# Optimization experiments

Hardware: AMD Instinct MI355X
Metric: run time of the kernel (lower is better)

Reference implementation:

```python
import jax, jax.numpy as jnp
import numpy as np
from jax import lax

PATCH = 4
EMBED = 96


def setup_inputs() -> dict:
    key = jax.random.key(0)
    k1, k2, k3, k4, k5 = jax.random.split(key, 5)
    rgb = jax.random.normal(k1, (8, 3, 512, 512), dtype=jnp.float32)
    hs = jax.random.normal(k2, (8, 4, 512, 512), dtype=jnp.float32)
    dem = jax.random.normal(k3, (8, 1, 512, 512), dtype=jnp.float32)
    W = jax.random.normal(k4, (EMBED, 1, PATCH, PATCH), dtype=jnp.float32) * 0.05
    b = jax.random.normal(k5, (EMBED,), dtype=jnp.float32) * 0.05
    return {"rgb": rgb, "hs": hs, "dem": dem, "W": W, "b": b}


def reference(rgb, hs, dem, W, b):
    # Concatenate modalities along channel dim: [B, C=8, H, Wd]
    x = jnp.concatenate([rgb, hs, dem], axis=1)
    B, C, H, Wd = x.shape
    # Pad H, W up to a multiple of patch size (right/bottom), as in _padding
    pad_h = (-H) % PATCH
    pad_w = (-Wd) % PATCH
    if pad_h or pad_w:
        x = jnp.pad(x, ((0, 0), (0, 0), (0, pad_h), (0, pad_w)))
    H2, W2 = x.shape[2], x.shape[3]
    # Each channel goes through the SAME 1->embed_dim conv; fold channels into batch
    xc = x.reshape(B * C, 1, H2, W2)
    y = lax.conv_general_dilated(
        xc, W,
        window_strides=(PATCH, PATCH),
        padding='VALID',
        dimension_numbers=('NCHW', 'OIHW', 'NCHW'),
    ) + b[None, :, None, None]
    Hp, Wp = y.shape[2], y.shape[3]
    # Unfold back and concat per-channel embeddings along channel dim: [B, C*embed, Hp, Wp]
    y = y.reshape(B, C * EMBED, Hp, Wp)
    return y
```

## Files before the change

### kernel.cpp

```cpp
#include <hip/hip_runtime.h>
#include <hip/hip_bf16.h>

#define PATCH 4
#define EMBED 96
#define HIN 512
#define WIN 512
#define HP 128
#define WP 128
#define BATCH 8
#define CHAN 8

__global__ __launch_bounds__(256, 4)
void patch_embed_kernel(const float* __restrict__ rgb,
                        const float* __restrict__ hs,
                        const float* __restrict__ dem,
                        const float* __restrict__ W,
                        const float* __restrict__ bias,
                        float* __restrict__ out) {
    const int blk = blockIdx.x;
    const int hp2 = blk & 63;
    const int bc  = blk >> 6;
    const int b   = bc >> 3;
    const int c   = bc & 7;

    const int tid = threadIdx.x;
    const int hp  = hp2 * 2 + (tid >> 7);
    const int wp  = tid & 127;

    const float* src;
    if (c < 3)      src = rgb + (size_t)(b * 3 + c)       * (HIN * WIN);
    else if (c < 7) src = hs  + (size_t)(b * 4 + (c - 3)) * (HIN * WIN);
    else            src = dem + (size_t)b                 * (HIN * WIN);

    const float* row0 = src + (size_t)(hp * PATCH) * WIN + wp * PATCH;
    const float4 p0 = *(const float4*)(row0);
    const float4 p1 = *(const float4*)(row0 + WIN);
    const float4 p2 = *(const float4*)(row0 + 2 * WIN);
    const float4 p3 = *(const float4*)(row0 + 3 * WIN);

    float* outp = out + (((size_t)(b * CHAN * EMBED + c * EMBED) * HP + hp) * WP + wp);

    #pragma unroll 4
    for (int e = 0; e < EMBED; ++e) {
        const float4 w0 = *(const float4*)(W + e * 16);
        const float4 w1 = *(const float4*)(W + e * 16 + 4);
        const float4 w2 = *(const float4*)(W + e * 16 + 8);
        const float4 w3 = *(const float4*)(W + e * 16 + 12);
        float acc = bias[e];
        acc = fmaf(p0.x, w0.x, acc); acc = fmaf(p0.y, w0.y, acc);
        acc = fmaf(p0.z, w0.z, acc); acc = fmaf(p0.w, w0.w, acc);
        acc = fmaf(p1.x, w1.x, acc); acc = fmaf(p1.y, w1.y, acc);
        acc = fmaf(p1.z, w1.z, acc); acc = fmaf(p1.w, w1.w, acc);
        acc = fmaf(p2.x, w2.x, acc); acc = fmaf(p2.y, w2.y, acc);
        acc = fmaf(p2.z, w2.z, acc); acc = fmaf(p2.w, w2.w, acc);
        acc = fmaf(p3.x, w3.x, acc); acc = fmaf(p3.y, w3.y, acc);
        acc = fmaf(p3.z, w3.z, acc); acc = fmaf(p3.w, w3.w, acc);
        outp[(size_t)e * (HP * WP)] = acc;
    }
}

extern "C" void kernel_launch(void* const* d_in, const int* in_sizes, int n_in,
                              void* d_out, int out_size, void* d_ws, size_t ws_size,
                              hipStream_t stream) {
    const float* rgb  = (const float*)d_in[0];
    const float* hs   = (const float*)d_in[1];
    const float* dem  = (const float*)d_in[2];
    const float* W    = (const float*)d_in[3];
    const float* bias = (const float*)d_in[4];
    float* out = (float*)d_out;

    const int grid = BATCH * CHAN * (HP / 2);
    patch_embed_kernel<<<grid, 256, 0, stream>>>(rgb, hs, dem, W, bias, out);
}
```

Before: 469.0 us.

## Compute four patches per thread with float4 stores and XCD-aware block mapping

Each thread now computes four adjacent output patches along the width, so it loads 16 float4 inputs and reuses each weight load four times. Output is written as float4, giving wider stores. Blocks now cover 8 patch rows, and the block index is remapped so the eight planes are spread across the XCDs in round-robin. The cost is more registers per thread and a grid four times smaller, which may lower occupancy in this store-bound kernel.

```diff
diff --git a/kernel.cpp b/kernel.cpp
--- a/kernel.cpp
+++ b/kernel.cpp
@@ -1,5 +1,4 @@
 #include <hip/hip_runtime.h>
-#include <hip/hip_bf16.h>
 
 #define PATCH 4
 #define EMBED 96
@@ -17,45 +16,61 @@
                         const float* __restrict__ W,
                         const float* __restrict__ bias,
                         float* __restrict__ out) {
-    const int blk = blockIdx.x;
-    const int hp2 = blk & 63;
-    const int bc  = blk >> 6;
-    const int b   = bc >> 3;
-    const int c   = bc & 7;
+    const int d     = blockIdx.x;
+    const int xcd   = d & 7;
+    const int j     = d >> 3;
+    const int plane = (j >> 4) * 8 + xcd;
+    const int hp8   = j & 15;
+    const int b = plane >> 3;
+    const int c = plane & 7;
 
     const int tid = threadIdx.x;
-    const int hp  = hp2 * 2 + (tid >> 7);
-    const int wp  = tid & 127;
+    const int hp  = hp8 * 8 + (tid >> 5);
+    const int wp4 = (tid & 31) * 4;
 
     const float* src;
     if (c < 3)      src = rgb + (size_t)(b * 3 + c)       * (HIN * WIN);
     else if (c < 7) src = hs  + (size_t)(b * 4 + (c - 3)) * (HIN * WIN);
     else            src = dem + (size_t)b                 * (HIN * WIN);
 
-    const float* row0 = src + (size_t)(hp * PATCH) * WIN + wp * PATCH;
-    const float4 p0 = *(const float4*)(row0);
-    const float4 p1 = *(const float4*)(row0 + WIN);
-    const float4 p2 = *(const float4*)(row0 + 2 * WIN);
-    const float4 p3 = *(const float4*)(row0 + 3 * WIN);
+    const float* base = src + (size_t)(hp * PATCH) * WIN + wp4 * PATCH;
 
-    float* outp = out + (((size_t)(b * CHAN * EMBED + c * EMBED) * HP + hp) * WP + wp);
+    float4 q[4][4];
+    #pragma unroll
+    for (int r = 0; r < 4; ++r) {
+        #pragma unroll
+        for (int k = 0; k < 4; ++k) {
+            q[r][k] = *(const float4*)(base + (size_t)r * WIN + k * PATCH);
+        }
+    }
 
-    #pragma unroll 4
+    float* outp = out + (((size_t)plane * EMBED * HP + hp) * WP + wp4);
+
+    #pragma unroll 2
     for (int e = 0; e < EMBED; ++e) {
-        const float4 w0 = *(const float4*)(W + e * 16);
-        const float4 w1 = *(const float4*)(W + e * 16 + 4);
-        const float4 w2 = *(const float4*)(W + e * 16 + 8);
-        const float4 w3 = *(const float4*)(W + e * 16 + 12);
-        float acc = bias[e];
-        acc = fmaf(p0.x, w0.x, acc); acc = fmaf(p0.y, w0.y, acc);
-        acc = fmaf(p0.z, w0.z, acc); acc = fmaf(p0.w, w0.w, acc);
-        acc = fmaf(p1.x, w1.x, acc); acc = fmaf(p1.y, w1.y, acc);
-        acc = fmaf(p1.z, w1.z, acc); acc = fmaf(p1.w, w1.w, acc);
-        acc = fmaf(p2.x, w2.x, acc); acc = fmaf(p2.y, w2.y, acc);
-        acc = fmaf(p2.z, w2.z, acc); acc = fmaf(p2.w, w2.w, acc);
-        acc = fmaf(p3.x, w3.x, acc); acc = fmaf(p3.y, w3.y, acc);
-        acc = fmaf(p3.z, w3.z, acc); acc = fmaf(p3.w, w3.w, acc);
-        outp[(size_t)e * (HP * WP)] = acc;
+        float4 w[4];
+        #pragma unroll
+        for (int r = 0; r < 4; ++r) {
+            w[r] = *(const float4*)(W + e * 16 + r * 4);
+        }
+        const float bb = bias[e];
+        float acc[4];
+        #pragma unroll
+        for (int k = 0; k < 4; ++k) acc[k] = bb;
+
+        #pragma unroll
+        for (int r = 0; r < 4; ++r) {
+            #pragma unroll
+            for (int k = 0; k < 4; ++k) {
+                acc[k] = fmaf(q[r][k].x, w[r].x, acc[k]);
+                acc[k] = fmaf(q[r][k].y, w[r].y, acc[k]);
+                acc[k] = fmaf(q[r][k].z, w[r].z, acc[k]);
+                acc[k] = fmaf(q[r][k].w, w[r].w, acc[k]);
+            }
+        }
+
+        *(float4*)(outp + (size_t)e * (HP * WP)) =
+            make_float4(acc[0], acc[1], acc[2], acc[3]);
     }
 }
 
@@ -69,6 +84,6 @@
     const float* bias = (const float*)d_in[4];
     float* out = (float*)d_out;
 
-    const int grid = BATCH * CHAN * (HP / 2);
+    const int grid = BATCH * CHAN * (HP / 8);
     patch_embed_kernel<<<grid, 256, 0, stream>>>(rgb, hs, dem, W, bias, out);
 }
```

New measurement: 642.8 us. 1.37x slower.
